# Kernel optimization log

Measured on AMD Instinct MI355X. Metric: run time of the kernel, lower is better.

The kernel has to match this reference:

```python
import jax, jax.numpy as jnp
import numpy as np

N = 128   # system size (number of sequential RNN steps)
B = 8192  # batch of samples
H = 128   # hidden units per layer (units=[128,128])
D = 2     # input_dim (spin up/down one-hot)


def setup_inputs() -> dict:
    key = jax.random.key(0)
    ks = jax.random.split(key, 11)
    s = 1.0 / np.sqrt(H)  # torch nn.RNNCell/Linear default U(-1/sqrt(H), 1/sqrt(H))
    bits = jax.random.randint(ks[0], (N, B), 0, D)
    samples = jax.nn.one_hot(bits, D, dtype=jnp.float32)  # (N, B, D) one-hot spins
    u = lambda k, shp: jax.random.uniform(k, shp, jnp.float32, -s, s)
    return {
        "samples": samples,
        "W_ih0": u(ks[1], (H, D)), "b_ih0": u(ks[2], (H,)),
        "W_hh0": u(ks[3], (H, H)), "b_hh0": u(ks[4], (H,)),
        "W_ih1": u(ks[5], (H, H)), "b_ih1": u(ks[6], (H,)),
        "W_hh1": u(ks[7], (H, H)), "b_hh1": u(ks[8], (H,)),
        "W_dense": u(ks[9], (D, H)), "b_dense": u(ks[10], (D,)),
    }


def reference(samples, W_ih0, b_ih0, W_hh0, b_hh0,
              W_ih1, b_ih1, W_hh1, b_hh1, W_dense, b_dense):
    # Faithful jax port of RNN_wavefunction.log_prob:
    # p_t = <softmax(dense(h1_t)), s_t>; returns sum_t log p_t with shape (1, B).
    # For one-hot s_t, log(sum(prob*s_t)) == sum(s_t * log_softmax(logits)) (stable form).
    Bsz = samples.shape[1]
    # input at step t is the sampled spin from step t-1; zeros at t=0
    inputs = jnp.concatenate(
        [jnp.zeros((1, Bsz, D), samples.dtype), samples[:-1]], axis=0)
    h0 = jnp.zeros((Bsz, H), samples.dtype)
    h1 = jnp.zeros((Bsz, H), samples.dtype)

    def step(carry, xs):
        h0, h1 = carry
        x_t, s_t = xs  # x_t: (B, D) prev spin one-hot, s_t: (B, D) current spin
        # nn.RNNCell: h' = tanh(x W_ih^T + b_ih + h W_hh^T + b_hh)
        h0 = jnp.tanh(x_t @ W_ih0.T + b_ih0 + h0 @ W_hh0.T + b_hh0)
        h1 = jnp.tanh(h0 @ W_ih1.T + b_ih1 + h1 @ W_hh1.T + b_hh1)
        logits = h1 @ W_dense.T + b_dense           # (B, 2)
        logp = jax.nn.log_softmax(logits, axis=-1)
        lp_t = jnp.sum(logp * s_t, axis=-1)          # (B,) = log p(s_t)
        return (h0, h1), lp_t

    _, lps = jax.lax.scan(step, (h0, h1), (inputs, samples))  # lps: (N, B)
    return jnp.sum(lps, axis=0, keepdims=True)  # (1, B), matches torch keepdim=True
```

## Files before the change

### kernel.cpp

```cpp
#include <hip/hip_runtime.h>
#include <hip/hip_bf16.h>


#define NSTEP 128
#define BTOT  8192
#define HID   128
#define MB    16
#define NBLK  (BTOT / MB)
#define NTHR  512

typedef __attribute__((ext_vector_type(8))) short bf16x8;
typedef __attribute__((ext_vector_type(4))) float f32x4;
typedef __attribute__((ext_vector_type(2))) float f32x2;
typedef __attribute__((ext_vector_type(2))) unsigned uint32x2;

__device__ __forceinline__ short f2bf(float v) {
    unsigned u = __builtin_bit_cast(unsigned, v);
    u += 0x7FFFu + ((u >> 16) & 1u);
    return (short)(u >> 16);
}
__device__ __forceinline__ unsigned cvt2bf(float a, float b) {
    __hip_bfloat162 h2 = __float22bfloat162_rn(make_float2(a, b));
    unsigned u; __builtin_memcpy(&u, &h2, sizeof(u));
    return u;
}
__device__ __forceinline__ f32x2 tanh2(f32x2 x) {
    f32x2 z = x * 2.885390081777927f;
    float e0 = __builtin_exp2f(z.x);
    float e1 = __builtin_exp2f(z.y);
    f32x2 d = {e0 + 1.0f, e1 + 1.0f};
    float r = __builtin_amdgcn_rcpf(d.x * d.y);
    f32x2 inv = {r * d.y, r * d.x};
    return inv * -2.0f + 1.0f;
}

__global__ __launch_bounds__(NTHR, 4) void rnn_wf_kernel(
    const float* __restrict__ samples,
    const float* __restrict__ Wih0,
    const float* __restrict__ bih0,
    const float* __restrict__ Whh0,
    const float* __restrict__ bhh0,
    const float* __restrict__ Wih1,
    const float* __restrict__ bih1,
    const float* __restrict__ Whh1,
    const float* __restrict__ bhh1,
    const float* __restrict__ Wd,
    const float* __restrict__ bd,
    float* __restrict__ out)
{
    __shared__ short sH0[2][MB * HID];
    __shared__ short sH1[2][MB * HID];
    __shared__ unsigned sMask[NSTEP];
    __shared__ float sLd[NSTEP * 17];
    __shared__ __attribute__((aligned(16))) float sBias[4 * HID];
    __shared__ __attribute__((aligned(16))) short sFwd[4 * 64 * 8];

    const int tid  = threadIdx.x;
    const int b0   = blockIdx.x * MB;
    const int w    = tid >> 6;
    const int lane = tid & 63;
    const int q    = lane >> 4;
    const int c    = lane & 15;

    if (tid < NSTEP) {
        unsigned msk = 0;
        #pragma unroll
        for (int m = 0; m < MB; ++m) {
            float e1 = samples[((size_t)tid * BTOT + b0 + m) * 2 + 1];
            if (e1 > 0.5f) msk |= (1u << m);
        }
        sMask[tid] = msk;
    }
    if (tid >= NSTEP && tid < NSTEP + HID) {
        const int n = tid - NSTEP;
        const float bb = bih0[n] + bhh0[n];
        sBias[n]       = bb + Wih0[n * 2 + 0];
        sBias[128 + n] = bb + Wih0[n * 2 + 1];
        sBias[256 + n] = bih1[n] + bhh1[n];
        sBias[384 + n] = bb;
    }
    if (tid >= 256 && tid < 512) {
        const int t2 = tid - 256;
        const int kb = t2 >> 6, l = t2 & 63, cc = l & 15, qq = l >> 4;
        bf16x8 v;
        #pragma unroll
        for (int j = 0; j < 8; ++j)
            v[j] = (cc < 2) ? f2bf(Wd[cc * HID + kb * 32 + qq * 8 + j]) : (short)0;
        *reinterpret_cast<bf16x8*>(&sFwd[(kb * 64 + l) * 8]) = v;
    }

    bf16x8 fhh0[4], fih1[4], fhh1[4];
    {
        const int nn = w * 16 + c;
        #pragma unroll
        for (int kb = 0; kb < 4; ++kb) {
            const int off = nn * HID + kb * 32 + q * 8;
            bf16x8 v0, v1, v2;
            #pragma unroll
            for (int j = 0; j < 8; ++j) {
                v0[j] = f2bf(Whh0[off + j]);
                v1[j] = f2bf(Wih1[off + j]);
                v2[j] = f2bf(Whh1[off + j]);
            }
            fhh0[kb] = v0; fih1[kb] = v1; fhh1[kb] = v2;
        }
    }
    const float bd0 = bd[0], bd1 = bd[1];

    int ra[4];
    #pragma unroll
    for (int kb = 0; kb < 4; ++kb)
        ra[kb] = c * HID + (((kb * 4 + q) ^ c) << 3);
    const int wa = c * HID + (((2 * w + (q >> 1)) ^ c) << 3) + ((q & 1) << 2);
    const int ib = w * 16 + q * 4;

    bool bmPrev = false;

    auto storeL = [&](short* buf, const f32x4& a) {
        f32x2 t0 = tanh2((f32x2){a[0], a[1]});
        f32x2 t1 = tanh2((f32x2){a[2], a[3]});
        uint32x2 v = {cvt2bf(t0.x, t0.y), cvt2bf(t1.x, t1.y)};
        *reinterpret_cast<uint32x2*>(&buf[wa]) = v;
    };

    __syncthreads();

    storeL(sH0[1], *reinterpret_cast<const f32x4*>(&sBias[384 + ib]));
    __syncthreads();

    {
        const bool bmIn = (sMask[0] >> c) & 1u;
        const float* bp = bmIn ? (sBias + 128) : sBias;
        f32x4 a0 = *reinterpret_cast<const f32x4*>(&bp[ib]);
        f32x4 a1 = *reinterpret_cast<const f32x4*>(&sBias[256 + ib]);
        #pragma unroll
        for (int kb = 0; kb < 4; ++kb) {
            bf16x8 f0 = *reinterpret_cast<const bf16x8*>(&sH0[1][ra[kb]]);
            a0 = __builtin_amdgcn_mfma_f32_16x16x32_bf16(fhh0[kb], f0, a0, 0, 0, 0);
            a1 = __builtin_amdgcn_mfma_f32_16x16x32_bf16(fih1[kb], f0, a1, 0, 0, 0);
        }
        storeL(sH0[0], a0);
        storeL(sH1[0], a1);
        bmPrev = bmIn;
        __syncthreads();
    }

    auto stepMain = [&](int i, const short* r0, const short* r1,
                        short* w0b, short* w1b) {
        const bool bmIn = (sMask[i - 1] >> c) & 1u;
        const float* bp = bmIn ? (sBias + 128) : sBias;
        f32x4 a0 = *reinterpret_cast<const f32x4*>(&bp[ib]);
        f32x4 a1 = *reinterpret_cast<const f32x4*>(&sBias[256 + ib]);
        bf16x8 f0[4], f1[4];
        #pragma unroll
        for (int kb = 0; kb < 4; ++kb) {
            f0[kb] = *reinterpret_cast<const bf16x8*>(&r0[ra[kb]]);
            f1[kb] = *reinterpret_cast<const bf16x8*>(&r1[ra[kb]]);
        }
        #pragma unroll
        for (int kb = 0; kb < 4; ++kb) {
            a0 = __builtin_amdgcn_mfma_f32_16x16x32_bf16(fhh0[kb], f0[kb], a0, 0, 0, 0);
            a1 = __builtin_amdgcn_mfma_f32_16x16x32_bf16(fhh1[kb], f1[kb], a1, 0, 0, 0);
        }
        #pragma unroll
        for (int kb = 0; kb < 4; ++kb)
            a1 = __builtin_amdgcn_mfma_f32_16x16x32_bf16(fih1[kb], f0[kb], a1, 0, 0, 0);
        if (w == (i & 7)) {
            f32x4 aL = {bd0, bd1, 0.f, 0.f};
            #pragma unroll
            for (int kb = 0; kb < 4; ++kb) {
                bf16x8 fw = *reinterpret_cast<const bf16x8*>(&sFwd[(kb * 64 + lane) * 8]);
                aL = __builtin_amdgcn_mfma_f32_16x16x32_bf16(fw, f1[kb], aL, 0, 0, 0);
            }
            if (q == 0)
                sLd[(i - 2) * 17 + c] = bmPrev ? (aL[0] - aL[1]) : (aL[1] - aL[0]);
        }
        bmPrev = bmIn;
        storeL(w0b, a0);
        storeL(w1b, a1);
        __syncthreads();
    };

    for (int i = 2; i < NSTEP; i += 2) {
        stepMain(i,     sH0[0], sH1[0], sH0[1], sH1[1]);
        stepMain(i + 1, sH0[1], sH1[1], sH0[0], sH1[0]);
    }

    {
        f32x4 a1 = *reinterpret_cast<const f32x4*>(&sBias[256 + ib]);
        bf16x8 f0[4], f1[4];
        #pragma unroll
        for (int kb = 0; kb < 4; ++kb) {
            f0[kb] = *reinterpret_cast<const bf16x8*>(&sH0[0][ra[kb]]);
            f1[kb] = *reinterpret_cast<const bf16x8*>(&sH1[0][ra[kb]]);
        }
        #pragma unroll
        for (int kb = 0; kb < 4; ++kb)
            a1 = __builtin_amdgcn_mfma_f32_16x16x32_bf16(fhh1[kb], f1[kb], a1, 0, 0, 0);
        #pragma unroll
        for (int kb = 0; kb < 4; ++kb)
            a1 = __builtin_amdgcn_mfma_f32_16x16x32_bf16(fih1[kb], f0[kb], a1, 0, 0, 0);
        if (w == 0) {
            f32x4 aL = {bd0, bd1, 0.f, 0.f};
            #pragma unroll
            for (int kb = 0; kb < 4; ++kb) {
                bf16x8 fw = *reinterpret_cast<const bf16x8*>(&sFwd[(kb * 64 + lane) * 8]);
                aL = __builtin_amdgcn_mfma_f32_16x16x32_bf16(fw, f1[kb], aL, 0, 0, 0);
            }
            if (q == 0)
                sLd[126 * 17 + c] = bmPrev ? (aL[0] - aL[1]) : (aL[1] - aL[0]);
        }
        storeL(sH1[1], a1);
        __syncthreads();
    }
    if (w == 1) {
        f32x4 aL = {bd0, bd1, 0.f, 0.f};
        #pragma unroll
        for (int kb = 0; kb < 4; ++kb) {
            bf16x8 f1 = *reinterpret_cast<const bf16x8*>(&sH1[1][ra[kb]]);
            bf16x8 fw = *reinterpret_cast<const bf16x8*>(&sFwd[(kb * 64 + lane) * 8]);
            aL = __builtin_amdgcn_mfma_f32_16x16x32_bf16(fw, f1, aL, 0, 0, 0);
        }
        if (q == 0) {
            const bool bit = (sMask[NSTEP - 1] >> c) & 1u;
            sLd[127 * 17 + c] = bit ? (aL[0] - aL[1]) : (aL[1] - aL[0]);
        }
    }
    __syncthreads();

    if (tid < 256) {
        const int s = tid >> 4;
        const int k = tid & 15;
        float acc = 0.0f;
        #pragma unroll
        for (int j = 0; j < 8; ++j) {
            const float x = sLd[(j * 16 + k) * 17 + s];
            const float ed = __builtin_exp2f(x * 1.4426950408889634f);
            acc -= 0.6931471805599453f * __builtin_log2f(1.0f + ed);
        }
        #pragma unroll
        for (int off = 1; off < 16; off <<= 1)
            acc += __shfl_xor(acc, off, 64);
        if (k == 0)
            out[b0 + s] = acc;
    }
}

extern "C" void kernel_launch(void* const* d_in, const int* in_sizes, int n_in,
                              void* d_out, int out_size, void* d_ws, size_t ws_size,
                              hipStream_t stream) {
    rnn_wf_kernel<<<NBLK, NTHR, 0, stream>>>(
        (const float*)d_in[0],
        (const float*)d_in[1],
        (const float*)d_in[2],
        (const float*)d_in[3],
        (const float*)d_in[4],
        (const float*)d_in[5],
        (const float*)d_in[6],
        (const float*)d_in[7],
        (const float*)d_in[8],
        (const float*)d_in[9],
        (const float*)d_in[10],
        (float*)d_out);
}
```

Baseline: 238.4 us.

## Shrink RNN block to two waves each owning four output tiles

The block goes from 8 waves to 2. Each wave now computes 64 hidden units (four 16-wide n-tiles), and all weight fragments, biases and dense weights are held in registers instead of shared memory. Per-step masks are pre-packed into per-lane bitmasks, and the layer-1 accumulation is split into two independent MFMA chains so more instructions can be in flight. The aim is to cut the per-step barrier cost and shared-memory traffic for bias and dense weights. The cost is much higher register pressure (48 weight fragments per lane) and fewer waves per block to hide latency.

```diff
diff --git a/kernel.cpp b/kernel.cpp
--- a/kernel.cpp
+++ b/kernel.cpp
@@ -7,7 +7,7 @@
 #define HID   128
 #define MB    16
 #define NBLK  (BTOT / MB)
-#define NTHR  512
+#define NTHR  128
 
 typedef __attribute__((ext_vector_type(8))) short bf16x8;
 typedef __attribute__((ext_vector_type(4))) float f32x4;
@@ -34,7 +34,7 @@
     return inv * -2.0f + 1.0f;
 }
 
-__global__ __launch_bounds__(NTHR, 4) void rnn_wf_kernel(
+__global__ __launch_bounds__(NTHR, 1) void rnn_wf_kernel(
     const float* __restrict__ samples,
     const float* __restrict__ Wih0,
     const float* __restrict__ bih0,
@@ -52,46 +52,28 @@
     __shared__ short sH1[2][MB * HID];
     __shared__ unsigned sMask[NSTEP];
     __shared__ float sLd[NSTEP * 17];
-    __shared__ __attribute__((aligned(16))) float sBias[4 * HID];
-    __shared__ __attribute__((aligned(16))) short sFwd[4 * 64 * 8];
 
     const int tid  = threadIdx.x;
     const int b0   = blockIdx.x * MB;
-    const int w    = tid >> 6;
+    const int W    = tid >> 6;
     const int lane = tid & 63;
     const int q    = lane >> 4;
     const int c    = lane & 15;
-
-    if (tid < NSTEP) {
+    const int nb   = W * 64;
+
+    {
         unsigned msk = 0;
-        #pragma unroll
         for (int m = 0; m < MB; ++m) {
             float e1 = samples[((size_t)tid * BTOT + b0 + m) * 2 + 1];
             if (e1 > 0.5f) msk |= (1u << m);
         }
         sMask[tid] = msk;
     }
-    if (tid >= NSTEP && tid < NSTEP + HID) {
-        const int n = tid - NSTEP;
-        const float bb = bih0[n] + bhh0[n];
-        sBias[n]       = bb + Wih0[n * 2 + 0];
-        sBias[128 + n] = bb + Wih0[n * 2 + 1];
-        sBias[256 + n] = bih1[n] + bhh1[n];
-        sBias[384 + n] = bb;
-    }
-    if (tid >= 256 && tid < 512) {
-        const int t2 = tid - 256;
-        const int kb = t2 >> 6, l = t2 & 63, cc = l & 15, qq = l >> 4;
-        bf16x8 v;
-        #pragma unroll
-        for (int j = 0; j < 8; ++j)
-            v[j] = (cc < 2) ? f2bf(Wd[cc * HID + kb * 32 + qq * 8 + j]) : (short)0;
-        *reinterpret_cast<bf16x8*>(&sFwd[(kb * 64 + l) * 8]) = v;
-    }
-
-    bf16x8 fhh0[4], fih1[4], fhh1[4];
-    {
-        const int nn = w * 16 + c;
+
+    bf16x8 fhh0[4][4], fih1[4][4], fhh1[4][4];
+    #pragma unroll
+    for (int nt = 0; nt < 4; ++nt) {
+        const int nn = nb + nt * 16 + c;
         #pragma unroll
         for (int kb = 0; kb < 4; ++kb) {
             const int off = nn * HID + kb * 32 + q * 8;
@@ -102,80 +84,124 @@
                 v1[j] = f2bf(Wih1[off + j]);
                 v2[j] = f2bf(Whh1[off + j]);
             }
-            fhh0[kb] = v0; fih1[kb] = v1; fhh1[kb] = v2;
-        }
-    }
+            fhh0[nt][kb] = v0; fih1[nt][kb] = v1; fhh1[nt][kb] = v2;
+        }
+    }
+    bf16x8 fwd[4];
+    #pragma unroll
+    for (int kb = 0; kb < 4; ++kb) {
+        bf16x8 v;
+        #pragma unroll
+        for (int j = 0; j < 8; ++j)
+            v[j] = (c < 2) ? f2bf(Wd[c * HID + kb * 32 + q * 8 + j]) : (short)0;
+        fwd[kb] = v;
+    }
+    f32x4 pA[4], pB[4], b1v[4], b0v[4];
+    #pragma unroll
+    for (int nt = 0; nt < 4; ++nt)
+        #pragma unroll
+        for (int r = 0; r < 4; ++r) {
+            const int n = nb + nt * 16 + q * 4 + r;
+            const float bb = bih0[n] + bhh0[n];
+            b0v[nt][r] = bb;
+            pA[nt][r]  = bb + Wih0[n * 2 + 0];
+            pB[nt][r]  = bb + Wih0[n * 2 + 1];
+            b1v[nt][r] = bih1[n] + bhh1[n];
+        }
     const float bd0 = bd[0], bd1 = bd[1];
 
     int ra[4];
     #pragma unroll
     for (int kb = 0; kb < 4; ++kb)
         ra[kb] = c * HID + (((kb * 4 + q) ^ c) << 3);
-    const int wa = c * HID + (((2 * w + (q >> 1)) ^ c) << 3) + ((q & 1) << 2);
-    const int ib = w * 16 + q * 4;
+    int wa[4];
+    #pragma unroll
+    for (int nt = 0; nt < 4; ++nt)
+        wa[nt] = c * HID + ((((W << 3) + (nt << 1) + (q >> 1)) ^ c) << 3)
+               + ((q & 1) << 2);
+
+    __syncthreads();
+
+    unsigned mw[4] = {0, 0, 0, 0};
+    for (int t = 0; t < NSTEP; ++t)
+        mw[t >> 5] |= ((sMask[t] >> c) & 1u) << (t & 31);
+
+    auto storeL = [&](short* buf, const f32x4* a) {
+        #pragma unroll
+        for (int nt = 0; nt < 4; ++nt) {
+            f32x2 t0 = tanh2((f32x2){a[nt][0], a[nt][1]});
+            f32x2 t1 = tanh2((f32x2){a[nt][2], a[nt][3]});
+            uint32x2 v = {cvt2bf(t0.x, t0.y), cvt2bf(t1.x, t1.y)};
+            *reinterpret_cast<uint32x2*>(&buf[wa[nt]]) = v;
+        }
+    };
 
     bool bmPrev = false;
 
-    auto storeL = [&](short* buf, const f32x4& a) {
-        f32x2 t0 = tanh2((f32x2){a[0], a[1]});
-        f32x2 t1 = tanh2((f32x2){a[2], a[3]});
-        uint32x2 v = {cvt2bf(t0.x, t0.y), cvt2bf(t1.x, t1.y)};
-        *reinterpret_cast<uint32x2*>(&buf[wa]) = v;
-    };
-
+    {
+        f32x4 a[4] = {b0v[0], b0v[1], b0v[2], b0v[3]};
+        storeL(sH0[1], a);
+    }
     __syncthreads();
 
-    storeL(sH0[1], *reinterpret_cast<const f32x4*>(&sBias[384 + ib]));
-    __syncthreads();
-
-    {
-        const bool bmIn = (sMask[0] >> c) & 1u;
-        const float* bp = bmIn ? (sBias + 128) : sBias;
-        f32x4 a0 = *reinterpret_cast<const f32x4*>(&bp[ib]);
-        f32x4 a1 = *reinterpret_cast<const f32x4*>(&sBias[256 + ib]);
-        #pragma unroll
-        for (int kb = 0; kb < 4; ++kb) {
-            bf16x8 f0 = *reinterpret_cast<const bf16x8*>(&sH0[1][ra[kb]]);
-            a0 = __builtin_amdgcn_mfma_f32_16x16x32_bf16(fhh0[kb], f0, a0, 0, 0, 0);
-            a1 = __builtin_amdgcn_mfma_f32_16x16x32_bf16(fih1[kb], f0, a1, 0, 0, 0);
+    {
+        const bool bm = mw[0] & 1u;
+        bf16x8 f0[4];
+        #pragma unroll
+        for (int kb = 0; kb < 4; ++kb)
+            f0[kb] = *reinterpret_cast<const bf16x8*>(&sH0[1][ra[kb]]);
+        f32x4 a0[4], a1[4];
+        #pragma unroll
+        for (int nt = 0; nt < 4; ++nt) {
+            a0[nt] = bm ? pB[nt] : pA[nt];
+            a1[nt] = b1v[nt];
+            #pragma unroll
+            for (int kb = 0; kb < 4; ++kb) {
+                a0[nt] = __builtin_amdgcn_mfma_f32_16x16x32_bf16(fhh0[nt][kb], f0[kb], a0[nt], 0, 0, 0);
+                a1[nt] = __builtin_amdgcn_mfma_f32_16x16x32_bf16(fih1[nt][kb], f0[kb], a1[nt], 0, 0, 0);
+            }
         }
         storeL(sH0[0], a0);
         storeL(sH1[0], a1);
-        bmPrev = bmIn;
+        bmPrev = bm;
         __syncthreads();
     }
 
     auto stepMain = [&](int i, const short* r0, const short* r1,
                         short* w0b, short* w1b) {
-        const bool bmIn = (sMask[i - 1] >> c) & 1u;
-        const float* bp = bmIn ? (sBias + 128) : sBias;
-        f32x4 a0 = *reinterpret_cast<const f32x4*>(&bp[ib]);
-        f32x4 a1 = *reinterpret_cast<const f32x4*>(&sBias[256 + ib]);
+        const bool bm = (mw[(i - 1) >> 5] >> ((i - 1) & 31)) & 1u;
         bf16x8 f0[4], f1[4];
         #pragma unroll
         for (int kb = 0; kb < 4; ++kb) {
             f0[kb] = *reinterpret_cast<const bf16x8*>(&r0[ra[kb]]);
             f1[kb] = *reinterpret_cast<const bf16x8*>(&r1[ra[kb]]);
         }
-        #pragma unroll
-        for (int kb = 0; kb < 4; ++kb) {
-            a0 = __builtin_amdgcn_mfma_f32_16x16x32_bf16(fhh0[kb], f0[kb], a0, 0, 0, 0);
-            a1 = __builtin_amdgcn_mfma_f32_16x16x32_bf16(fhh1[kb], f1[kb], a1, 0, 0, 0);
-        }
-        #pragma unroll
-        for (int kb = 0; kb < 4; ++kb)
-            a1 = __builtin_amdgcn_mfma_f32_16x16x32_bf16(fih1[kb], f0[kb], a1, 0, 0, 0);
-        if (w == (i & 7)) {
+        f32x4 a0[4], a1a[4], a1b[4];
+        #pragma unroll
+        for (int nt = 0; nt < 4; ++nt) {
+            a0[nt]  = bm ? pB[nt] : pA[nt];
+            a1a[nt] = b1v[nt];
+            a1b[nt] = {0.f, 0.f, 0.f, 0.f};
+            #pragma unroll
+            for (int kb = 0; kb < 4; ++kb) {
+                a0[nt]  = __builtin_amdgcn_mfma_f32_16x16x32_bf16(fhh0[nt][kb], f0[kb], a0[nt],  0, 0, 0);
+                a1a[nt] = __builtin_amdgcn_mfma_f32_16x16x32_bf16(fhh1[nt][kb], f1[kb], a1a[nt], 0, 0, 0);
+                a1b[nt] = __builtin_amdgcn_mfma_f32_16x16x32_bf16(fih1[nt][kb], f0[kb], a1b[nt], 0, 0, 0);
+            }
+        }
+        if (W == (i & 1)) {
             f32x4 aL = {bd0, bd1, 0.f, 0.f};
             #pragma unroll
-            for (int kb = 0; kb < 4; ++kb) {
-                bf16x8 fw = *reinterpret_cast<const bf16x8*>(&sFwd[(kb * 64 + lane) * 8]);
-                aL = __builtin_amdgcn_mfma_f32_16x16x32_bf16(fw, f1[kb], aL, 0, 0, 0);
-            }
+            for (int kb = 0; kb < 4; ++kb)
+                aL = __builtin_amdgcn_mfma_f32_16x16x32_bf16(fwd[kb], f1[kb], aL, 0, 0, 0);
             if (q == 0)
                 sLd[(i - 2) * 17 + c] = bmPrev ? (aL[0] - aL[1]) : (aL[1] - aL[0]);
         }
-        bmPrev = bmIn;
+        bmPrev = bm;
+        f32x4 a1[4];
+        #pragma unroll
+        for (int nt = 0; nt < 4; ++nt)
+            a1[nt] = a1a[nt] + a1b[nt];
         storeL(w0b, a0);
         storeL(w1b, a1);
         __syncthreads();
@@ -187,59 +213,64 @@
     }
 
     {
-        f32x4 a1 = *reinterpret_cast<const f32x4*>(&sBias[256 + ib]);
         bf16x8 f0[4], f1[4];
         #pragma unroll
         for (int kb = 0; kb < 4; ++kb) {
             f0[kb] = *reinterpret_cast<const bf16x8*>(&sH0[0][ra[kb]]);
             f1[kb] = *reinterpret_cast<const bf16x8*>(&sH1[0][ra[kb]]);
         }
-        #pragma unroll
-        for (int kb = 0; kb < 4; ++kb)
-            a1 = __builtin_amdgcn_mfma_f32_16x16x32_bf16(fhh1[kb], f1[kb], a1, 0, 0, 0);
-        #pragma unroll
-        for (int kb = 0; kb < 4; ++kb)
-            a1 = __builtin_amdgcn_mfma_f32_16x16x32_bf16(fih1[kb], f0[kb], a1, 0, 0, 0);
-        if (w == 0) {
+        f32x4 a1a[4], a1b[4];
+        #pragma unroll
+        for (int nt = 0; nt < 4; ++nt) {
+            a1a[nt] = b1v[nt];
+            a1b[nt] = {0.f, 0.f, 0.f, 0.f};
+            #pragma unroll
+            for (int kb = 0; kb < 4; ++kb) {
+                a1a[nt] = __builtin_amdgcn_mfma_f32_16x16x32_bf16(fhh1[nt][kb], f1[kb], a1a[nt], 0, 0, 0);
+                a1b[nt] = __builtin_amdgcn_mfma_f32_16x16x32_bf16(fih1[nt][kb], f0[kb], a1b[nt], 0, 0, 0);
+            }
+        }
+        if (W == 0) {
             f32x4 aL = {bd0, bd1, 0.f, 0.f};
             #pragma unroll
-            for (int kb = 0; kb < 4; ++kb) {
-                bf16x8 fw = *reinterpret_cast<const bf16x8*>(&sFwd[(kb * 64 + lane) * 8]);
-                aL = __builtin_amdgcn_mfma_f32_16x16x32_bf16(fw, f1[kb], aL, 0, 0, 0);
-            }
+            for (int kb = 0; kb < 4; ++kb)
+                aL = __builtin_amdgcn_mfma_f32_16x16x32_bf16(fwd[kb], f1[kb], aL, 0, 0, 0);
             if (q == 0)
                 sLd[126 * 17 + c] = bmPrev ? (aL[0] - aL[1]) : (aL[1] - aL[0]);
         }
+        f32x4 a1[4];
+        #pragma unroll
+        for (int nt = 0; nt < 4; ++nt)
+            a1[nt] = a1a[nt] + a1b[nt];
         storeL(sH1[1], a1);
         __syncthreads();
     }
-    if (w == 1) {
+    if (W == 1) {
         f32x4 aL = {bd0, bd1, 0.f, 0.f};
         #pragma unroll
         for (int kb = 0; kb < 4; ++kb) {
             bf16x8 f1 = *reinterpret_cast<const bf16x8*>(&sH1[1][ra[kb]]);
-            bf16x8 fw = *reinterpret_cast<const bf16x8*>(&sFwd[(kb * 64 + lane) * 8]);
-            aL = __builtin_amdgcn_mfma_f32_16x16x32_bf16(fw, f1, aL, 0, 0, 0);
+            aL = __builtin_amdgcn_mfma_f32_16x16x32_bf16(fwd[kb], f1, aL, 0, 0, 0);
         }
         if (q == 0) {
-            const bool bit = (sMask[NSTEP - 1] >> c) & 1u;
+            const bool bit = (mw[3] >> 31) & 1u;
             sLd[127 * 17 + c] = bit ? (aL[0] - aL[1]) : (aL[1] - aL[0]);
         }
     }
     __syncthreads();
 
-    if (tid < 256) {
-        const int s = tid >> 4;
-        const int k = tid & 15;
+    {
+        const int s = tid >> 3;
+        const int k = tid & 7;
         float acc = 0.0f;
         #pragma unroll
-        for (int j = 0; j < 8; ++j) {
-            const float x = sLd[(j * 16 + k) * 17 + s];
+        for (int j = 0; j < 16; ++j) {
+            const float x = sLd[(j * 8 + k) * 17 + s];
             const float ed = __builtin_exp2f(x * 1.4426950408889634f);
             acc -= 0.6931471805599453f * __builtin_log2f(1.0f + ed);
         }
         #pragma unroll
-        for (int off = 1; off < 16; off <<= 1)
+        for (int off = 1; off < 8; off <<= 1)
             acc += __shfl_xor(acc, off, 64);
         if (k == 0)
             out[b0 + s] = acc;
```

Result: slower. 323.5 us (+35.7%).

## Process two 16-row batch tiles per block to amortize weight fragments and barriers

Applied to the files above, without the earlier changes.

Each block now handles 32 samples as two 16-row MFMA tiles. This reuses the register-resident weight fragments across both tiles and halves the number of per-step barriers per sample. The biases and dense weights move from shared memory into registers, and sample bits are packed into per-lane bitmasks. Log-prob accumulation is done inline per wave, and the layer-1 sum is split into two independent accumulator chains. The cost is higher register pressure, reduced to 2 blocks per CU in the launch bounds, and only 256 blocks in the grid, which risks lower occupancy and latency hiding.

```diff
diff --git a/kernel.cpp b/kernel.cpp
--- a/kernel.cpp
+++ b/kernel.cpp
@@ -5,9 +5,10 @@
 #define NSTEP 128
 #define BTOT  8192
 #define HID   128
-#define MB    16
+#define MB    32
 #define NBLK  (BTOT / MB)
 #define NTHR  512
+#define MOFF  (16 * HID)
 
 typedef __attribute__((ext_vector_type(8))) short bf16x8;
 typedef __attribute__((ext_vector_type(4))) float f32x4;
@@ -34,7 +35,7 @@
     return inv * -2.0f + 1.0f;
 }
 
-__global__ __launch_bounds__(NTHR, 4) void rnn_wf_kernel(
+__global__ __launch_bounds__(NTHR, 2) void rnn_wf_kernel(
     const float* __restrict__ samples,
     const float* __restrict__ Wih0,
     const float* __restrict__ bih0,
@@ -51,9 +52,7 @@
     __shared__ short sH0[2][MB * HID];
     __shared__ short sH1[2][MB * HID];
     __shared__ unsigned sMask[NSTEP];
-    __shared__ float sLd[NSTEP * 17];
-    __shared__ __attribute__((aligned(16))) float sBias[4 * HID];
-    __shared__ __attribute__((aligned(16))) short sFwd[4 * 64 * 8];
+    __shared__ float sLp[8 * MB];
 
     const int tid  = threadIdx.x;
     const int b0   = blockIdx.x * MB;
@@ -71,23 +70,6 @@
         }
         sMask[tid] = msk;
     }
-    if (tid >= NSTEP && tid < NSTEP + HID) {
-        const int n = tid - NSTEP;
-        const float bb = bih0[n] + bhh0[n];
-        sBias[n]       = bb + Wih0[n * 2 + 0];
-        sBias[128 + n] = bb + Wih0[n * 2 + 1];
-        sBias[256 + n] = bih1[n] + bhh1[n];
-        sBias[384 + n] = bb;
-    }
-    if (tid >= 256 && tid < 512) {
-        const int t2 = tid - 256;
-        const int kb = t2 >> 6, l = t2 & 63, cc = l & 15, qq = l >> 4;
-        bf16x8 v;
-        #pragma unroll
-        for (int j = 0; j < 8; ++j)
-            v[j] = (cc < 2) ? f2bf(Wd[cc * HID + kb * 32 + qq * 8 + j]) : (short)0;
-        *reinterpret_cast<bf16x8*>(&sFwd[(kb * 64 + l) * 8]) = v;
-    }
 
     bf16x8 fhh0[4], fih1[4], fhh1[4];
     {
@@ -104,6 +86,25 @@
             }
             fhh0[kb] = v0; fih1[kb] = v1; fhh1[kb] = v2;
         }
+    }
+    bf16x8 fwd[4];
+    #pragma unroll
+    for (int kb = 0; kb < 4; ++kb) {
+        bf16x8 v;
+        #pragma unroll
+        for (int j = 0; j < 8; ++j)
+            v[j] = (c < 2) ? f2bf(Wd[c * HID + kb * 32 + q * 8 + j]) : (short)0;
+        fwd[kb] = v;
+    }
+    f32x4 pA, pB, b1v, b0v;
+    #pragma unroll
+    for (int r = 0; r < 4; ++r) {
+        const int n = w * 16 + q * 4 + r;
+        const float bb = bih0[n] + bhh0[n];
+        b0v[r] = bb;
+        pA[r]  = bb + Wih0[n * 2 + 0];
+        pB[r]  = bb + Wih0[n * 2 + 1];
+        b1v[r] = bih1[n] + bhh1[n];
     }
     const float bd0 = bd[0], bd1 = bd[1];
 
@@ -112,72 +113,100 @@
     for (int kb = 0; kb < 4; ++kb)
         ra[kb] = c * HID + (((kb * 4 + q) ^ c) << 3);
     const int wa = c * HID + (((2 * w + (q >> 1)) ^ c) << 3) + ((q & 1) << 2);
-    const int ib = w * 16 + q * 4;
-
-    bool bmPrev = false;
-
-    auto storeL = [&](short* buf, const f32x4& a) {
+
+    __syncthreads();
+
+    unsigned mw0[4] = {0,0,0,0}, mw1[4] = {0,0,0,0};
+    for (int t = 0; t < NSTEP; ++t) {
+        const unsigned mk = sMask[t];
+        mw0[t >> 5] |= ((mk >> c)        & 1u) << (t & 31);
+        mw1[t >> 5] |= ((mk >> (16 + c)) & 1u) << (t & 31);
+    }
+    auto mbit = [&](const unsigned* mw, int t) -> bool {
+        return (mw[t >> 5] >> (t & 31)) & 1u;
+    };
+
+    float lp0 = 0.0f, lp1 = 0.0f;
+
+    auto storeOne = [&](short* buf, int mt, const f32x4& a) {
         f32x2 t0 = tanh2((f32x2){a[0], a[1]});
         f32x2 t1 = tanh2((f32x2){a[2], a[3]});
         uint32x2 v = {cvt2bf(t0.x, t0.y), cvt2bf(t1.x, t1.y)};
-        *reinterpret_cast<uint32x2*>(&buf[wa]) = v;
-    };
-
+        *reinterpret_cast<uint32x2*>(&buf[mt * MOFF + wa]) = v;
+    };
+    auto duty = [&](const bf16x8* f1m, const unsigned* mwm, int t, float& acc) {
+        f32x4 aL = {bd0, bd1, 0.f, 0.f};
+        #pragma unroll
+        for (int kb = 0; kb < 4; ++kb)
+            aL = __builtin_amdgcn_mfma_f32_16x16x32_bf16(fwd[kb], f1m[kb], aL, 0, 0, 0);
+        const bool bit = mbit(mwm, t);
+        const float diff = bit ? (aL[0] - aL[1]) : (aL[1] - aL[0]);
+        const float ed = __builtin_exp2f(diff * 1.4426950408889634f);
+        acc -= 0.6931471805599453f * __builtin_log2f(1.0f + ed);
+    };
+
+    storeOne(sH0[1], 0, b0v);
+    storeOne(sH0[1], 1, b0v);
     __syncthreads();
 
-    storeL(sH0[1], *reinterpret_cast<const f32x4*>(&sBias[384 + ib]));
-    __syncthreads();
-
-    {
-        const bool bmIn = (sMask[0] >> c) & 1u;
-        const float* bp = bmIn ? (sBias + 128) : sBias;
-        f32x4 a0 = *reinterpret_cast<const f32x4*>(&bp[ib]);
-        f32x4 a1 = *reinterpret_cast<const f32x4*>(&sBias[256 + ib]);
-        #pragma unroll
-        for (int kb = 0; kb < 4; ++kb) {
-            bf16x8 f0 = *reinterpret_cast<const bf16x8*>(&sH0[1][ra[kb]]);
-            a0 = __builtin_amdgcn_mfma_f32_16x16x32_bf16(fhh0[kb], f0, a0, 0, 0, 0);
-            a1 = __builtin_amdgcn_mfma_f32_16x16x32_bf16(fih1[kb], f0, a1, 0, 0, 0);
-        }
-        storeL(sH0[0], a0);
-        storeL(sH1[0], a1);
-        bmPrev = bmIn;
+    {
+        bf16x8 f0[2][4];
+        #pragma unroll
+        for (int mt = 0; mt < 2; ++mt)
+            #pragma unroll
+            for (int kb = 0; kb < 4; ++kb)
+                f0[mt][kb] = *reinterpret_cast<const bf16x8*>(&sH0[1][mt * MOFF + ra[kb]]);
+        f32x4 a0[2], a1[2];
+        a0[0] = mbit(mw0, 0) ? pB : pA;
+        a0[1] = mbit(mw1, 0) ? pB : pA;
+        a1[0] = b1v; a1[1] = b1v;
+        #pragma unroll
+        for (int mt = 0; mt < 2; ++mt)
+            #pragma unroll
+            for (int kb = 0; kb < 4; ++kb) {
+                a0[mt] = __builtin_amdgcn_mfma_f32_16x16x32_bf16(fhh0[kb], f0[mt][kb], a0[mt], 0, 0, 0);
+                a1[mt] = __builtin_amdgcn_mfma_f32_16x16x32_bf16(fih1[kb], f0[mt][kb], a1[mt], 0, 0, 0);
+            }
+        #pragma unroll
+        for (int mt = 0; mt < 2; ++mt) {
+            storeOne(sH0[0], mt, a0[mt]);
+            storeOne(sH1[0], mt, a1[mt]);
+        }
         __syncthreads();
     }
 
     auto stepMain = [&](int i, const short* r0, const short* r1,
                         short* w0b, short* w1b) {
-        const bool bmIn = (sMask[i - 1] >> c) & 1u;
-        const float* bp = bmIn ? (sBias + 128) : sBias;
-        f32x4 a0 = *reinterpret_cast<const f32x4*>(&bp[ib]);
-        f32x4 a1 = *reinterpret_cast<const f32x4*>(&sBias[256 + ib]);
-        bf16x8 f0[4], f1[4];
-        #pragma unroll
-        for (int kb = 0; kb < 4; ++kb) {
-            f0[kb] = *reinterpret_cast<const bf16x8*>(&r0[ra[kb]]);
-            f1[kb] = *reinterpret_cast<const bf16x8*>(&r1[ra[kb]]);
-        }
-        #pragma unroll
-        for (int kb = 0; kb < 4; ++kb) {
-            a0 = __builtin_amdgcn_mfma_f32_16x16x32_bf16(fhh0[kb], f0[kb], a0, 0, 0, 0);
-            a1 = __builtin_amdgcn_mfma_f32_16x16x32_bf16(fhh1[kb], f1[kb], a1, 0, 0, 0);
-        }
-        #pragma unroll
-        for (int kb = 0; kb < 4; ++kb)
-            a1 = __builtin_amdgcn_mfma_f32_16x16x32_bf16(fih1[kb], f0[kb], a1, 0, 0, 0);
-        if (w == (i & 7)) {
-            f32x4 aL = {bd0, bd1, 0.f, 0.f};
-            #pragma unroll
-            for (int kb = 0; kb < 4; ++kb) {
-                bf16x8 fw = *reinterpret_cast<const bf16x8*>(&sFwd[(kb * 64 + lane) * 8]);
-                aL = __builtin_amdgcn_mfma_f32_16x16x32_bf16(fw, f1[kb], aL, 0, 0, 0);
-            }
-            if (q == 0)
-                sLd[(i - 2) * 17 + c] = bmPrev ? (aL[0] - aL[1]) : (aL[1] - aL[0]);
-        }
-        bmPrev = bmIn;
-        storeL(w0b, a0);
-        storeL(w1b, a1);
+        const int ip = i - 1;
+        bf16x8 f0[2][4], f1[2][4];
+        #pragma unroll
+        for (int mt = 0; mt < 2; ++mt)
+            #pragma unroll
+            for (int kb = 0; kb < 4; ++kb) {
+                f0[mt][kb] = *reinterpret_cast<const bf16x8*>(&r0[mt * MOFF + ra[kb]]);
+                f1[mt][kb] = *reinterpret_cast<const bf16x8*>(&r1[mt * MOFF + ra[kb]]);
+            }
+        f32x4 a0[2], a1a[2], a1b[2];
+        a0[0]  = mbit(mw0, ip) ? pB : pA;
+        a0[1]  = mbit(mw1, ip) ? pB : pA;
+        a1a[0] = b1v; a1a[1] = b1v;
+        a1b[0] = {0.f,0.f,0.f,0.f}; a1b[1] = {0.f,0.f,0.f,0.f};
+        #pragma unroll
+        for (int mt = 0; mt < 2; ++mt)
+            #pragma unroll
+            for (int kb = 0; kb < 4; ++kb) {
+                a0[mt]  = __builtin_amdgcn_mfma_f32_16x16x32_bf16(fhh0[kb], f0[mt][kb], a0[mt],  0, 0, 0);
+                a1a[mt] = __builtin_amdgcn_mfma_f32_16x16x32_bf16(fhh1[kb], f1[mt][kb], a1a[mt], 0, 0, 0);
+                a1b[mt] = __builtin_amdgcn_mfma_f32_16x16x32_bf16(fih1[kb], f0[mt][kb], a1b[mt], 0, 0, 0);
+            }
+        if (w == (i & 7))       duty(f1[0], mw0, i - 2, lp0);
+        if (w == ((i + 4) & 7)) duty(f1[1], mw1, i - 2, lp1);
+        #pragma unroll
+        for (int mt = 0; mt < 2; ++mt) {
+            storeOne(w0b, mt, a0[mt]);
+            f32x4 a1 = a1a[mt] + a1b[mt];
+            storeOne(w1b, mt, a1);
+        }
         __syncthreads();
     };
 
@@ -187,62 +216,61 @@
     }
 
     {
-        f32x4 a1 = *reinterpret_cast<const f32x4*>(&sBias[256 + ib]);
-        bf16x8 f0[4], f1[4];
-        #pragma unroll
-        for (int kb = 0; kb < 4; ++kb) {
-            f0[kb] = *reinterpret_cast<const bf16x8*>(&sH0[0][ra[kb]]);
-            f1[kb] = *reinterpret_cast<const bf16x8*>(&sH1[0][ra[kb]]);
-        }
-        #pragma unroll
-        for (int kb = 0; kb < 4; ++kb)
-            a1 = __builtin_amdgcn_mfma_f32_16x16x32_bf16(fhh1[kb], f1[kb], a1, 0, 0, 0);
-        #pragma unroll
-        for (int kb = 0; kb < 4; ++kb)
-            a1 = __builtin_amdgcn_mfma_f32_16x16x32_bf16(fih1[kb], f0[kb], a1, 0, 0, 0);
-        if (w == 0) {
-            f32x4 aL = {bd0, bd1, 0.f, 0.f};
-            #pragma unroll
-            for (int kb = 0; kb < 4; ++kb) {
-                bf16x8 fw = *reinterpret_cast<const bf16x8*>(&sFwd[(kb * 64 + lane) * 8]);
-                aL = __builtin_amdgcn_mfma_f32_16x16x32_bf16(fw, f1[kb], aL, 0, 0, 0);
-            }
-            if (q == 0)
-                sLd[126 * 17 + c] = bmPrev ? (aL[0] - aL[1]) : (aL[1] - aL[0]);
-        }
-        storeL(sH1[1], a1);
+        bf16x8 f0[2][4], f1[2][4];
+        #pragma unroll
+        for (int mt = 0; mt < 2; ++mt)
+            #pragma unroll
+            for (int kb = 0; kb < 4; ++kb) {
+                f0[mt][kb] = *reinterpret_cast<const bf16x8*>(&sH0[0][mt * MOFF + ra[kb]]);
+                f1[mt][kb] = *reinterpret_cast<const bf16x8*>(&sH1[0][mt * MOFF + ra[kb]]);
+            }
+        f32x4 a1a[2], a1b[2];
+        a1a[0] = b1v; a1a[1] = b1v;
+        a1b[0] = {0.f,0.f,0.f,0.f}; a1b[1] = {0.f,0.f,0.f,0.f};
+        #pragma unroll
+        for (int mt = 0; mt < 2; ++mt)
+            #pragma unroll
+            for (int kb = 0; kb < 4; ++kb) {
+                a1a[mt] = __builtin_amdgcn_mfma_f32_16x16x32_bf16(fhh1[kb], f1[mt][kb], a1a[mt], 0, 0, 0);
+                a1b[mt] = __builtin_amdgcn_mfma_f32_16x16x32_bf16(fih1[kb], f0[mt][kb], a1b[mt], 0, 0, 0);
+            }
+        if (w == 0) duty(f1[0], mw0, 126, lp0);
+        if (w == 4) duty(f1[1], mw1, 126, lp1);
+        #pragma unroll
+        for (int mt = 0; mt < 2; ++mt) {
+            f32x4 a1 = a1a[mt] + a1b[mt];
+            storeOne(sH1[1], mt, a1);
+        }
         __syncthreads();
     }
-    if (w == 1) {
-        f32x4 aL = {bd0, bd1, 0.f, 0.f};
-        #pragma unroll
-        for (int kb = 0; kb < 4; ++kb) {
-            bf16x8 f1 = *reinterpret_cast<const bf16x8*>(&sH1[1][ra[kb]]);
-            bf16x8 fw = *reinterpret_cast<const bf16x8*>(&sFwd[(kb * 64 + lane) * 8]);
-            aL = __builtin_amdgcn_mfma_f32_16x16x32_bf16(fw, f1, aL, 0, 0, 0);
-        }
-        if (q == 0) {
-            const bool bit = (sMask[NSTEP - 1] >> c) & 1u;
-            sLd[127 * 17 + c] = bit ? (aL[0] - aL[1]) : (aL[1] - aL[0]);
-        }
+    {
+        if (w == 1) {
+            bf16x8 f1[4];
+            #pragma unroll
+            for (int kb = 0; kb < 4; ++kb)
+                f1[kb] = *reinterpret_cast<const bf16x8*>(&sH1[1][ra[kb]]);
+            duty(f1, mw0, 127, lp0);
+        }
+        if (w == 5) {
+            bf16x8 f1[4];
+            #pragma unroll
+            for (int kb = 0; kb < 4; ++kb)
+                f1[kb] = *reinterpret_cast<const bf16x8*>(&sH1[1][MOFF + ra[kb]]);
+            duty(f1, mw1, 127, lp1);
+        }
+    }
+
+    if (q == 0) {
+        sLp[w * MB + c]      = lp0;
+        sLp[w * MB + 16 + c] = lp1;
     }
     __syncthreads();
-
-    if (tid < 256) {
-        const int s = tid >> 4;
-        const int k = tid & 15;
-        float acc = 0.0f;
-        #pragma unroll
-        for (int j = 0; j < 8; ++j) {
-            const float x = sLd[(j * 16 + k) * 17 + s];
-            const float ed = __builtin_exp2f(x * 1.4426950408889634f);
-            acc -= 0.6931471805599453f * __builtin_log2f(1.0f + ed);
-        }
-        #pragma unroll
-        for (int off = 1; off < 16; off <<= 1)
-            acc += __shfl_xor(acc, off, 64);
-        if (k == 0)
-            out[b0 + s] = acc;
+    if (tid < MB) {
+        float s = 0.0f;
+        #pragma unroll
+        for (int ww = 0; ww < 8; ++ww)
+            s += sLp[ww * MB + tid];
+        out[b0 + tid] = s;
     }
 }
 
```

Measured after the change: 260.9 us. 1.09x slower.
